# Kernel tuning notes

Hardware: AMD Instinct MI355X
Metric: run time of the kernel (lower is better)

The kernel has to match this reference:

```python
import jax, jax.numpy as jnp
import numpy as np

N_NODES = 100000
N_EDGES = 1600000
D_IN = 128
D_OUT = 64
K_HOPS = 2


def setup_inputs() -> dict:
    key = jax.random.key(0)
    k1, k2, k3, k4, k5, k6, k7 = jax.random.split(key, 7)
    x = jax.random.normal(k1, (N_NODES, D_IN), dtype=jnp.float32)
    edge_index = jax.random.randint(k2, (2, N_EDGES), 0, N_NODES, dtype=jnp.int32)
    edge_weight = jax.random.uniform(k3, (N_EDGES,), dtype=jnp.float32)
    W1 = jax.random.normal(k4, (D_IN, D_IN), dtype=jnp.float32) * (1.0 / np.sqrt(D_IN))
    b1 = jax.random.normal(k5, (D_IN,), dtype=jnp.float32) * 0.01
    W2 = jax.random.normal(k6, (D_IN, D_OUT), dtype=jnp.float32) * (1.0 / np.sqrt(D_IN))
    b2 = jax.random.normal(k7, (D_OUT,), dtype=jnp.float32) * 0.01
    return {"x": x, "edge_index": edge_index, "edge_weight": edge_weight,
            "is_cluster": 0, "W1": W1, "b1": b1, "W2": W2, "b2": b2}


def reference(x, edge_index, edge_weight, is_cluster, W1, b1, W2, b2):
    # K-hop weighted sparse propagation: x <- scatter_add(x[src] * w, dst)
    src, dst = edge_index[0], edge_index[1]
    n = x.shape[0]
    for _ in range(K_HOPS):
        msgs = x[src] * edge_weight[:, None]          # [E, D] gather
        x = jax.ops.segment_sum(msgs, dst, num_segments=n)  # [N, D] scatter
    # transform (non-cluster path): lin1 -> relu -> lin2 -> log_softmax
    h = jax.nn.relu(x @ W1 + b1)
    logits = h @ W2 + b2
    return jax.nn.log_softmax(logits, axis=1)
```

## Files before the change

kernel.cpp:

```cpp
#include <hip/hip_runtime.h>
#include <cstdint>
#include <cstddef>

#define NN 100000
#define NE 1600000
#define D_IN 128
#define D_OUT 64
#define NB_BKT 391
#define BKT_CAP 4608
#define TILE 8192

typedef __attribute__((ext_vector_type(8))) short bf16x8;
typedef __attribute__((ext_vector_type(4))) float f32x4;

__device__ __forceinline__ float bflo(unsigned u) {
    union { unsigned u; float f; } x; x.u = u << 16; return x.f;
}
__device__ __forceinline__ float bfhi(unsigned u) {
    union { unsigned u; float f; } x; x.u = u & 0xffff0000u; return x.f;
}
__device__ __forceinline__ unsigned f2b(float f) {
    union { float f; unsigned u; } x; x.f = f;
    unsigned u = x.u + 0x7fffu + ((x.u >> 16) & 1u);
    return u >> 16;
}

__device__ __forceinline__ void fma8(float* acc, uint4 v, float w) {
    acc[0] = fmaf(w, bflo(v.x), acc[0]);
    acc[1] = fmaf(w, bfhi(v.x), acc[1]);
    acc[2] = fmaf(w, bflo(v.y), acc[2]);
    acc[3] = fmaf(w, bfhi(v.y), acc[3]);
    acc[4] = fmaf(w, bflo(v.z), acc[4]);
    acc[5] = fmaf(w, bfhi(v.z), acc[5]);
    acc[6] = fmaf(w, bflo(v.w), acc[6]);
    acc[7] = fmaf(w, bfhi(v.w), acc[7]);
}

__global__ void __launch_bounds__(256) fill_p1(
        const int* __restrict__ src, const int* __restrict__ dst,
        const float* __restrict__ w, int* __restrict__ gcur,
        int2* __restrict__ gbuf, int E) {
    __shared__ int cnt[NB_BKT];
    __shared__ int base[NB_BKT];
    int tid = threadIdx.x;
    int t0 = blockIdx.x * TILE;
    int t1 = min(t0 + TILE, E);
    for (int i = tid; i < NB_BKT; i += 256) cnt[i] = 0;
    __syncthreads();
    for (int e = t0 + tid; e < t1; e += 256)
        atomicAdd(&cnt[dst[e] >> 8], 1);
    __syncthreads();
    for (int i = tid; i < NB_BKT; i += 256) {
        int c = cnt[i];
        base[i] = c ? (i * BKT_CAP + atomicAdd(&gcur[i], c)) : 0;
        cnt[i] = 0;
    }
    __syncthreads();
    for (int e = t0 + tid; e < t1; e += 256) {
        int d = dst[e];
        int b = d >> 8;
        int r = atomicAdd(&cnt[b], 1);
        int pos = base[b] + r;
        if (pos < (b + 1) * BKT_CAP) {
            unsigned u = (unsigned)src[e] | ((unsigned)(d & 255) << 17);
            gbuf[pos] = make_int2((int)u, __float_as_int(w[e]));
        }
    }
}

__global__ void __launch_bounds__(256) fill_p2(
        const int2* __restrict__ gbuf, const int* __restrict__ gcur,
        int2* __restrict__ rownfo, unsigned* __restrict__ epk, int n) {
    __shared__ int2 sg[BKT_CAP];
    __shared__ unsigned se[BKT_CAP];
    __shared__ int cnt[256];
    __shared__ int lofs[256];
    __shared__ int pcnt[256];
    int tid = threadIdx.x;
    int bucket = blockIdx.x;
    int node0 = bucket << 8;
    int beg = bucket * BKT_CAP;
    int m = min(gcur[bucket], BKT_CAP);
    cnt[tid] = 0;
    pcnt[tid] = 0;
    __syncthreads();
    for (int i = tid; i < m; i += 256) {
        int2 p = gbuf[beg + i];
        sg[i] = p;
        atomicAdd(&cnt[(unsigned)p.x >> 17], 1);
    }
    __syncthreads();
    int v = cnt[tid];
    lofs[tid] = v;
    __syncthreads();
    for (int off = 1; off < 256; off <<= 1) {
        int t = (tid >= off) ? lofs[tid - off] : 0;
        __syncthreads();
        lofs[tid] += t;
        __syncthreads();
    }
    int myofs = lofs[tid] - v;
    __syncthreads();
    lofs[tid] = myofs;
    __syncthreads();
    for (int i = tid; i < m; i += 256) {
        int2 p = sg[i];
        unsigned u = (unsigned)p.x;
        int local = (int)(u >> 17);
        unsigned w15 = (unsigned)(__int_as_float(p.y) * 32767.0f + 0.5f);
        int r = atomicAdd(&pcnt[local], 1);
        se[lofs[local] + r] = (u & 0x1FFFFu) | (w15 << 17);
    }
    __syncthreads();
    {
        unsigned* a = se + myofs;
        for (int i = 1; i < v; ++i) {
            unsigned val = a[i];
            unsigned key = val & 0x1FFFFu;
            int j = i - 1;
            while (j >= 0 && (a[j] & 0x1FFFFu) > key) { a[j + 1] = a[j]; --j; }
            a[j + 1] = val;
        }
    }
    __syncthreads();
    for (int i = tid; i < m; i += 256) epk[beg + i] = se[i];
    int node = node0 + tid;
    if (node < n) rownfo[node] = make_int2(beg + myofs, beg + myofs + v);
}

__global__ void conv_x(const float4* __restrict__ in, uint4* __restrict__ out, int n8) {
    int i = blockIdx.x * blockDim.x + threadIdx.x;
    if (i >= n8) return;
    float4 a = in[(size_t)i * 2], b = in[(size_t)i * 2 + 1];
    uint4 o;
    o.x = f2b(a.x) | (f2b(a.y) << 16);
    o.y = f2b(a.z) | (f2b(a.w) << 16);
    o.z = f2b(b.x) | (f2b(b.y) << 16);
    o.w = f2b(b.z) | (f2b(b.w) << 16);
    out[i] = o;
}

__global__ void prep_w(const float* __restrict__ W1, const float* __restrict__ W2,
                       char* __restrict__ wt) {
    int tid = blockIdx.x * blockDim.x + threadIdx.x;
    if (tid < 128 * 32) {
        int ch = tid >> 5, kq = tid & 31;
        unsigned lo = f2b(W1[(kq * 4 + 0) * 128 + ch]) | (f2b(W1[(kq * 4 + 1) * 128 + ch]) << 16);
        unsigned hi = f2b(W1[(kq * 4 + 2) * 128 + ch]) | (f2b(W1[(kq * 4 + 3) * 128 + ch]) << 16);
        *(uint2*)(wt + ch * 256 + kq * 8) = make_uint2(lo, hi);
    } else if (tid < 128 * 32 + 64 * 32) {
        int t = tid - 128 * 32;
        int ch = t >> 5, kq = t & 31;
        unsigned lo = f2b(W2[(kq * 4 + 0) * 64 + ch]) | (f2b(W2[(kq * 4 + 1) * 64 + ch]) << 16);
        unsigned hi = f2b(W2[(kq * 4 + 2) * 64 + ch]) | (f2b(W2[(kq * 4 + 3) * 64 + ch]) << 16);
        *(uint2*)(wt + 32768 + ch * 256 + kq * 8) = make_uint2(lo, hi);
    }
}

__global__ void __launch_bounds__(256) prop_b(
        const uint4* __restrict__ xin, uint4* __restrict__ xout,
        const int2* __restrict__ rownfo, const unsigned* __restrict__ epk, int n) {
    int wid = (blockIdx.x * 256 + threadIdx.x) >> 6;
    if (wid >= n) return;
    int lane = threadIdx.x & 63;
    int q = lane >> 4, c = lane & 15;
    int2 be = rownfo[wid];
    int beg = be.x, end = be.y;
    const float ws = 1.0f / 32767.0f;
    float acc[8] = {0.f, 0.f, 0.f, 0.f, 0.f, 0.f, 0.f, 0.f};
    int e = beg + q;
    for (; e + 12 < end; e += 16) {
        unsigned p0 = epk[e];
        unsigned p1 = epk[e + 4];
        unsigned p2 = epk[e + 8];
        unsigned p3 = epk[e + 12];
        uint4 v0 = xin[(size_t)(p0 & 0x1FFFFu) * 16 + c];
        uint4 v1 = xin[(size_t)(p1 & 0x1FFFFu) * 16 + c];
        uint4 v2 = xin[(size_t)(p2 & 0x1FFFFu) * 16 + c];
        uint4 v3 = xin[(size_t)(p3 & 0x1FFFFu) * 16 + c];
        fma8(acc, v0, (float)(p0 >> 17) * ws);
        fma8(acc, v1, (float)(p1 >> 17) * ws);
        fma8(acc, v2, (float)(p2 >> 17) * ws);
        fma8(acc, v3, (float)(p3 >> 17) * ws);
    }
    if (e + 4 < end) {
        unsigned p0 = epk[e];
        unsigned p1 = epk[e + 4];
        uint4 v0 = xin[(size_t)(p0 & 0x1FFFFu) * 16 + c];
        uint4 v1 = xin[(size_t)(p1 & 0x1FFFFu) * 16 + c];
        fma8(acc, v0, (float)(p0 >> 17) * ws);
        fma8(acc, v1, (float)(p1 >> 17) * ws);
        e += 8;
    }
    if (e < end) {
        unsigned p0 = epk[e];
        uint4 v0 = xin[(size_t)(p0 & 0x1FFFFu) * 16 + c];
        fma8(acc, v0, (float)(p0 >> 17) * ws);
    }
    #pragma unroll
    for (int i = 0; i < 8; ++i) {
        acc[i] += __shfl_xor(acc[i], 16);
        acc[i] += __shfl_xor(acc[i], 32);
    }
    if (q == 0) {
        uint4 o;
        o.x = f2b(acc[0]) | (f2b(acc[1]) << 16);
        o.y = f2b(acc[2]) | (f2b(acc[3]) << 16);
        o.z = f2b(acc[4]) | (f2b(acc[5]) << 16);
        o.w = f2b(acc[6]) | (f2b(acc[7]) << 16);
        xout[(size_t)wid * 16 + c] = o;
    }
}

__global__ void __launch_bounds__(256) mlp_mfma(
        const unsigned short* __restrict__ y2b, const char* __restrict__ wt,
        const float* __restrict__ b1, const float* __restrict__ b2,
        float* __restrict__ out, int n) {
    __shared__ char lds[32768];
    int tid = threadIdx.x;
    int wave = tid >> 6, lane = tid & 63;
    int c = lane & 15, g = lane >> 4;
    int nb = blockIdx.x * 128 + wave * 32;
    char* ht = lds + wave * 8192;

    f32x4 acc[2][8];
    #pragma unroll
    for (int t = 0; t < 8; ++t) {
        float bv = b1[t * 16 + c];
        f32x4 v = {bv, bv, bv, bv};
        acc[0][t] = v; acc[1][t] = v;
    }
    #pragma unroll
    for (int ks = 0; ks < 4; ++ks) {
        bf16x8 a[2];
        #pragma unroll
        for (int r = 0; r < 2; ++r) {
            int row = nb + r * 16 + c;
            if (row >= n) row = n - 1;
            a[r] = *(const bf16x8*)(y2b + (size_t)row * 128 + ks * 32 + g * 8);
        }
        #pragma unroll
        for (int t = 0; t < 8; ++t) {
            int ch = t * 16 + c;
            bf16x8 b = *(const bf16x8*)(wt + ch * 256 + ks * 64 + g * 16);
            acc[0][t] = __builtin_amdgcn_mfma_f32_16x16x32_bf16(a[0], b, acc[0][t], 0, 0, 0);
            acc[1][t] = __builtin_amdgcn_mfma_f32_16x16x32_bf16(a[1], b, acc[1][t], 0, 0, 0);
        }
    }
    #pragma unroll
    for (int r = 0; r < 2; ++r) {
        #pragma unroll
        for (int t = 0; t < 8; ++t) {
            int ch = t * 16 + c;
            unsigned lo = f2b(fmaxf(acc[r][t][0], 0.f)) | (f2b(fmaxf(acc[r][t][1], 0.f)) << 16);
            unsigned hi = f2b(fmaxf(acc[r][t][2], 0.f)) | (f2b(fmaxf(acc[r][t][3], 0.f)) << 16);
            *(uint2*)(ht + ch * 64 + (r * 16 + g * 4) * 2) = make_uint2(lo, hi);
        }
    }
    __syncthreads();

    f32x4 g2[4][2];
    #pragma unroll
    for (int T = 0; T < 4; ++T) {
        float4 bb = *(const float4*)(b2 + T * 16 + g * 4);
        f32x4 v = {bb.x, bb.y, bb.z, bb.w};
        g2[T][0] = v; g2[T][1] = v;
    }
    #pragma unroll
    for (int ks = 0; ks < 4; ++ks) {
        bf16x8 aw[4];
        #pragma unroll
        for (int T = 0; T < 4; ++T) {
            int oc = T * 16 + c;
            aw[T] = *(const bf16x8*)(wt + 32768 + oc * 256 + ks * 64 + g * 16);
        }
        bf16x8 hb[2];
        #pragma unroll
        for (int p = 0; p < 2; ++p) {
            #pragma unroll
            for (int j = 0; j < 8; ++j) {
                int k = ks * 32 + g * 8 + j;
                hb[p][j] = *(const short*)(ht + k * 64 + (p * 16 + c) * 2);
            }
        }
        #pragma unroll
        for (int T = 0; T < 4; ++T) {
            #pragma unroll
            for (int p = 0; p < 2; ++p)
                g2[T][p] = __builtin_amdgcn_mfma_f32_16x16x32_bf16(aw[T], hb[p], g2[T][p], 0, 0, 0);
        }
    }

    #pragma unroll
    for (int p = 0; p < 2; ++p) {
        int node = nb + p * 16 + c;
        float m = -1e30f;
        #pragma unroll
        for (int T = 0; T < 4; ++T)
            #pragma unroll
            for (int j = 0; j < 4; ++j) m = fmaxf(m, g2[T][p][j]);
        m = fmaxf(m, __shfl_xor(m, 16));
        m = fmaxf(m, __shfl_xor(m, 32));
        float s = 0.f;
        #pragma unroll
        for (int T = 0; T < 4; ++T)
            #pragma unroll
            for (int j = 0; j < 4; ++j) s += __expf(g2[T][p][j] - m);
        s += __shfl_xor(s, 16);
        s += __shfl_xor(s, 32);
        float lse = m + __logf(s);
        if (node < n) {
            #pragma unroll
            for (int T = 0; T < 4; ++T) {
                float4 o = make_float4(g2[T][p][0] - lse, g2[T][p][1] - lse,
                                       g2[T][p][2] - lse, g2[T][p][3] - lse);
                *(float4*)(out + (size_t)node * 64 + T * 16 + g * 4) = o;
            }
        }
    }
}

extern "C" void kernel_launch(void* const* d_in, const int* in_sizes, int n_in,
                              void* d_out, int out_size, void* d_ws, size_t ws_size,
                              hipStream_t stream) {
    const float* x  = (const float*)d_in[0];
    const int*   ei = (const int*)  d_in[1];
    const float* w  = (const float*)d_in[2];
    const float* W1 = (const float*)d_in[4];
    const float* b1 = (const float*)d_in[5];
    const float* W2 = (const float*)d_in[6];
    const float* b2 = (const float*)d_in[7];
    float* out = (float*)d_out;

    const int n = NN, E = NE;
    const int* src = ei;
    const int* dst = ei + E;

    char* ws = (char*)d_ws;
    size_t off = 0;
    auto alloc = [&](size_t bytes) {
        char* p = ws + off;
        off += (bytes + 15) & ~(size_t)15;
        return p;
    };
    int*      gcur   = (int*)     alloc((size_t)NB_BKT * 4);
    int2*     rownfo = (int2*)    alloc((size_t)NN * 8);
    unsigned* epk    = (unsigned*)alloc((size_t)NB_BKT * BKT_CAP * 4);
    uint4*    xb     = (uint4*)   alloc((size_t)NN * D_IN * 2);
    uint4*    y1b    = (uint4*)   alloc((size_t)NN * D_IN * 2);
    uint4*    y2b    = (uint4*)   alloc((size_t)NN * D_IN * 2);
    char*     wt     = (char*)    alloc(49152);
    int2*     gbuf   = (int2*)y2b;

    int n8 = n * D_IN / 8;
    conv_x<<<(n8 + 255) / 256, 256, 0, stream>>>((const float4*)x, xb, n8);
    prep_w<<<(6144 + 255) / 256, 256, 0, stream>>>(W1, W2, wt);

    hipMemsetAsync(gcur, 0, (size_t)NB_BKT * 4, stream);
    int ntile = (E + TILE - 1) / TILE;
    fill_p1<<<ntile, 256, 0, stream>>>(src, dst, w, gcur, gbuf, E);
    fill_p2<<<NB_BKT, 256, 0, stream>>>(gbuf, gcur, rownfo, epk, n);

    int pblocks = (n * 64 + 255) / 256;
    prop_b<<<pblocks, 256, 0, stream>>>(xb,  y1b, rownfo, epk, n);
    prop_b<<<pblocks, 256, 0, stream>>>(y1b, y2b, rownfo, epk, n);

    mlp_mfma<<<(n + 127) / 128, 256, 0, stream>>>((const unsigned short*)y2b, wt,
                                                  b1, b2, out, n);
}
```

Baseline: 296.5 us.

## Add source-chunked sliding-window propagation kernel for cache locality of gathers

Edges within each destination row are now grouped by 8192-node source chunk via a 16-bin counting sort in fill_p2, which replaces the per-row insertion sort, and per-(node, chunk) segment descriptors are written out. A new prop_sw kernel processes the first 98304 nodes chunk by chunk, so concurrently running waves gather from the same source window and reuse L2 cache. Remaining tail nodes still go through prop_b. Risks include extra segment metadata traffic, per-segment counts clamped at 255, loop divergence across the three rows a wave handles, and lower per-wave parallelism.

```diff
diff --git a/kernel.cpp b/kernel.cpp
--- a/kernel.cpp
+++ b/kernel.cpp
@@ -9,6 +9,8 @@
 #define NB_BKT 391
 #define BKT_CAP 4608
 #define TILE 8192
+#define NCH 13
+#define SWN 98304
 
 typedef __attribute__((ext_vector_type(8))) short bf16x8;
 typedef __attribute__((ext_vector_type(4))) float f32x4;
@@ -70,62 +72,57 @@
 
 __global__ void __launch_bounds__(256) fill_p2(
         const int2* __restrict__ gbuf, const int* __restrict__ gcur,
-        int2* __restrict__ rownfo, unsigned* __restrict__ epk, int n) {
+        unsigned* __restrict__ segs2, int2* __restrict__ rownfo,
+        unsigned* __restrict__ epk, int n) {
     __shared__ int2 sg[BKT_CAP];
-    __shared__ unsigned se[BKT_CAP];
-    __shared__ int cnt[256];
-    __shared__ int lofs[256];
-    __shared__ int pcnt[256];
+    __shared__ int cnt[256 * 16];
+    __shared__ int sc[256];
     int tid = threadIdx.x;
     int bucket = blockIdx.x;
-    int node0 = bucket << 8;
-    int beg = bucket * BKT_CAP;
+    int base = bucket * BKT_CAP;
     int m = min(gcur[bucket], BKT_CAP);
-    cnt[tid] = 0;
-    pcnt[tid] = 0;
+    for (int i = tid; i < 4096; i += 256) cnt[i] = 0;
     __syncthreads();
     for (int i = tid; i < m; i += 256) {
-        int2 p = gbuf[beg + i];
+        int2 p = gbuf[base + i];
         sg[i] = p;
-        atomicAdd(&cnt[(unsigned)p.x >> 17], 1);
-    }
-    __syncthreads();
-    int v = cnt[tid];
-    lofs[tid] = v;
+        unsigned u = (unsigned)p.x;
+        atomicAdd(&cnt[((u >> 17) << 4) + ((u & 0x1FFFFu) >> 13)], 1);
+    }
+    __syncthreads();
+    int mycnt[16];
+    int s = 0;
+    #pragma unroll
+    for (int c = 0; c < 16; ++c) { mycnt[c] = cnt[tid * 16 + c]; s += mycnt[c]; }
+    sc[tid] = s;
     __syncthreads();
     for (int off = 1; off < 256; off <<= 1) {
-        int t = (tid >= off) ? lofs[tid - off] : 0;
+        int t = (tid >= off) ? sc[tid - off] : 0;
         __syncthreads();
-        lofs[tid] += t;
+        sc[tid] += t;
         __syncthreads();
     }
-    int myofs = lofs[tid] - v;
-    __syncthreads();
-    lofs[tid] = myofs;
+    int running = sc[tid] - s;
+    int node = (bucket << 8) + tid;
+    int start0 = base + running;
+    #pragma unroll
+    for (int c = 0; c < 16; ++c) {
+        cnt[tid * 16 + c] = running;
+        if (c < NCH && node < SWN)
+            segs2[(size_t)((node >> 13) * NCH + c) * 8192 + (node & 8191)] =
+                ((unsigned)(base + running) << 8) | (unsigned)min(mycnt[c], 255);
+        running += mycnt[c];
+    }
+    if (node < n) rownfo[node] = make_int2(start0, start0 + s);
     __syncthreads();
     for (int i = tid; i < m; i += 256) {
         int2 p = sg[i];
         unsigned u = (unsigned)p.x;
-        int local = (int)(u >> 17);
+        int bin = (int)((u >> 17) << 4) + (int)((u & 0x1FFFFu) >> 13);
         unsigned w15 = (unsigned)(__int_as_float(p.y) * 32767.0f + 0.5f);
-        int r = atomicAdd(&pcnt[local], 1);
-        se[lofs[local] + r] = (u & 0x1FFFFu) | (w15 << 17);
-    }
-    __syncthreads();
-    {
-        unsigned* a = se + myofs;
-        for (int i = 1; i < v; ++i) {
-            unsigned val = a[i];
-            unsigned key = val & 0x1FFFFu;
-            int j = i - 1;
-            while (j >= 0 && (a[j] & 0x1FFFFu) > key) { a[j + 1] = a[j]; --j; }
-            a[j + 1] = val;
-        }
-    }
-    __syncthreads();
-    for (int i = tid; i < m; i += 256) epk[beg + i] = se[i];
-    int node = node0 + tid;
-    if (node < n) rownfo[node] = make_int2(beg + myofs, beg + myofs + v);
+        int r = atomicAdd(&cnt[bin], 1);
+        epk[base + r] = (u & 0x1FFFFu) | (w15 << 17);
+    }
 }
 
 __global__ void conv_x(const float4* __restrict__ in, uint4* __restrict__ out, int n8) {
@@ -157,40 +154,79 @@
     }
 }
 
+__global__ void __launch_bounds__(256, 8) prop_sw(
+        const uint4* __restrict__ xin, uint4* __restrict__ xout,
+        const unsigned* __restrict__ segs2, const unsigned* __restrict__ epk) {
+    int wid = (blockIdx.x * 256 + threadIdx.x) >> 6;
+    int lane = threadIdx.x & 63;
+    int q = lane >> 4, c16 = lane & 15;
+    const float ws = 1.0f / 32767.0f;
+    float acc0[8] = {0.f,0.f,0.f,0.f,0.f,0.f,0.f,0.f};
+    float acc1[8] = {0.f,0.f,0.f,0.f,0.f,0.f,0.f,0.f};
+    float acc2[8] = {0.f,0.f,0.f,0.f,0.f,0.f,0.f,0.f};
+    for (int c = 0; c < NCH; ++c) {
+        unsigned s0 = segs2[(size_t)((q     ) * NCH + c) * 8192 + wid];
+        unsigned s1 = segs2[(size_t)((4 + q) * NCH + c) * 8192 + wid];
+        unsigned s2 = segs2[(size_t)((8 + q) * NCH + c) * 8192 + wid];
+        int e0 = (int)(s0 >> 8), n0 = (int)(s0 & 255u);
+        int e1 = (int)(s1 >> 8), n1 = (int)(s1 & 255u);
+        int e2 = (int)(s2 >> 8), n2 = (int)(s2 & 255u);
+        int rmax = max(n0, max(n1, n2));
+        unsigned p0 = 0, p1 = 0, p2 = 0;
+        if (n0 > 0) p0 = epk[e0];
+        if (n1 > 0) p1 = epk[e1];
+        if (n2 > 0) p2 = epk[e2];
+        for (int r = 0; r < rmax; ++r) {
+            uint4 v0 = {0,0,0,0}, v1 = {0,0,0,0}, v2 = {0,0,0,0};
+            float w0 = 0.f, w1 = 0.f, w2 = 0.f;
+            if (r < n0) { v0 = xin[(size_t)(p0 & 0x1FFFFu) * 16 + c16]; w0 = (float)(p0 >> 17) * ws; }
+            if (r < n1) { v1 = xin[(size_t)(p1 & 0x1FFFFu) * 16 + c16]; w1 = (float)(p1 >> 17) * ws; }
+            if (r < n2) { v2 = xin[(size_t)(p2 & 0x1FFFFu) * 16 + c16]; w2 = (float)(p2 >> 17) * ws; }
+            if (r + 1 < n0) p0 = epk[e0 + r + 1];
+            if (r + 1 < n1) p1 = epk[e1 + r + 1];
+            if (r + 1 < n2) p2 = epk[e2 + r + 1];
+            fma8(acc0, v0, w0);
+            fma8(acc1, v1, w1);
+            fma8(acc2, v2, w2);
+        }
+    }
+    uint4 o;
+    o.x = f2b(acc0[0]) | (f2b(acc0[1]) << 16);
+    o.y = f2b(acc0[2]) | (f2b(acc0[3]) << 16);
+    o.z = f2b(acc0[4]) | (f2b(acc0[5]) << 16);
+    o.w = f2b(acc0[6]) | (f2b(acc0[7]) << 16);
+    xout[(size_t)(wid + (q     ) * 8192) * 16 + c16] = o;
+    o.x = f2b(acc1[0]) | (f2b(acc1[1]) << 16);
+    o.y = f2b(acc1[2]) | (f2b(acc1[3]) << 16);
+    o.z = f2b(acc1[4]) | (f2b(acc1[5]) << 16);
+    o.w = f2b(acc1[6]) | (f2b(acc1[7]) << 16);
+    xout[(size_t)(wid + (4 + q) * 8192) * 16 + c16] = o;
+    o.x = f2b(acc2[0]) | (f2b(acc2[1]) << 16);
+    o.y = f2b(acc2[2]) | (f2b(acc2[3]) << 16);
+    o.z = f2b(acc2[4]) | (f2b(acc2[5]) << 16);
+    o.w = f2b(acc2[6]) | (f2b(acc2[7]) << 16);
+    xout[(size_t)(wid + (8 + q) * 8192) * 16 + c16] = o;
+}
+
 __global__ void __launch_bounds__(256) prop_b(
         const uint4* __restrict__ xin, uint4* __restrict__ xout,
         const int2* __restrict__ rownfo, const unsigned* __restrict__ epk, int n) {
-    int wid = (blockIdx.x * 256 + threadIdx.x) >> 6;
+    int wid = SWN + ((blockIdx.x * 256 + threadIdx.x) >> 6);
     if (wid >= n) return;
     int lane = threadIdx.x & 63;
     int q = lane >> 4, c = lane & 15;
     int2 be = rownfo[wid];
     int beg = be.x, end = be.y;
     const float ws = 1.0f / 32767.0f;
-    float acc[8] = {0.f, 0.f, 0.f, 0.f, 0.f, 0.f, 0.f, 0.f};
+    float acc[8] = {0.f,0.f,0.f,0.f,0.f,0.f,0.f,0.f};
     int e = beg + q;
-    for (; e + 12 < end; e += 16) {
-        unsigned p0 = epk[e];
-        unsigned p1 = epk[e + 4];
-        unsigned p2 = epk[e + 8];
-        unsigned p3 = epk[e + 12];
-        uint4 v0 = xin[(size_t)(p0 & 0x1FFFFu) * 16 + c];
-        uint4 v1 = xin[(size_t)(p1 & 0x1FFFFu) * 16 + c];
-        uint4 v2 = xin[(size_t)(p2 & 0x1FFFFu) * 16 + c];
-        uint4 v3 = xin[(size_t)(p3 & 0x1FFFFu) * 16 + c];
-        fma8(acc, v0, (float)(p0 >> 17) * ws);
-        fma8(acc, v1, (float)(p1 >> 17) * ws);
-        fma8(acc, v2, (float)(p2 >> 17) * ws);
-        fma8(acc, v3, (float)(p3 >> 17) * ws);
-    }
-    if (e + 4 < end) {
+    for (; e + 4 < end; e += 8) {
         unsigned p0 = epk[e];
         unsigned p1 = epk[e + 4];
         uint4 v0 = xin[(size_t)(p0 & 0x1FFFFu) * 16 + c];
         uint4 v1 = xin[(size_t)(p1 & 0x1FFFFu) * 16 + c];
         fma8(acc, v0, (float)(p0 >> 17) * ws);
         fma8(acc, v1, (float)(p1 >> 17) * ws);
-        e += 8;
     }
     if (e < end) {
         unsigned p0 = epk[e];
@@ -344,6 +380,7 @@
         return p;
     };
     int*      gcur   = (int*)     alloc((size_t)NB_BKT * 4);
+    unsigned* segs2  = (unsigned*)alloc((size_t)12 * NCH * 8192 * 4);
     int2*     rownfo = (int2*)    alloc((size_t)NN * 8);
     unsigned* epk    = (unsigned*)alloc((size_t)NB_BKT * BKT_CAP * 4);
     uint4*    xb     = (uint4*)   alloc((size_t)NN * D_IN * 2);
@@ -359,11 +396,13 @@
     hipMemsetAsync(gcur, 0, (size_t)NB_BKT * 4, stream);
     int ntile = (E + TILE - 1) / TILE;
     fill_p1<<<ntile, 256, 0, stream>>>(src, dst, w, gcur, gbuf, E);
-    fill_p2<<<NB_BKT, 256, 0, stream>>>(gbuf, gcur, rownfo, epk, n);
-
-    int pblocks = (n * 64 + 255) / 256;
-    prop_b<<<pblocks, 256, 0, stream>>>(xb,  y1b, rownfo, epk, n);
-    prop_b<<<pblocks, 256, 0, stream>>>(y1b, y2b, rownfo, epk, n);
+    fill_p2<<<NB_BKT, 256, 0, stream>>>(gbuf, gcur, segs2, rownfo, epk, n);
+
+    int tail_blocks = ((n - SWN) * 64 + 255) / 256;
+    prop_sw<<<2048, 256, 0, stream>>>(xb,  y1b, segs2, epk);
+    prop_b <<<tail_blocks, 256, 0, stream>>>(xb,  y1b, rownfo, epk, n);
+    prop_sw<<<2048, 256, 0, stream>>>(y1b, y2b, segs2, epk);
+    prop_b <<<tail_blocks, 256, 0, stream>>>(y1b, y2b, rownfo, epk, n);
 
     mlp_mfma<<<(n + 127) / 128, 256, 0, stream>>>((const unsigned short*)y2b, wt,
                                                   b1, b2, out, n);
```

Measured after the change: 268.4 us. 1.1x faster.
